# Optimization experiments

Measured on AMD Instinct MI355X. Metric: run time of the kernel, lower is better.

## Reference

```python
import jax, jax.numpy as jnp
import numpy as np

HIDDEN = 1024
HEADS = 16
HEAD = HIDDEN // HEADS


def setup_inputs() -> dict:
    key = jax.random.key(0)
    ks = jax.random.split(key, 6)
    B, T = 2, 2048
    x = jax.random.normal(ks[0], (B, T, HIDDEN), dtype=jnp.float32)
    mask = jnp.ones((T, T), dtype=jnp.float32)
    s = 1.0 / np.sqrt(HIDDEN)
    Wqkv = jax.random.normal(ks[1], (HIDDEN, 3 * HIDDEN), dtype=jnp.float32) * s
    bqkv = jnp.zeros((3 * HIDDEN,), dtype=jnp.float32)
    Wproj = jax.random.normal(ks[2], (HIDDEN, HIDDEN), dtype=jnp.float32) * s
    bproj = jnp.zeros((HIDDEN,), dtype=jnp.float32)
    return {"x": x, "mask": mask, "Wqkv": Wqkv, "bqkv": bqkv,
            "Wproj": Wproj, "bproj": bproj}


def reference(x, mask, Wqkv, bqkv, Wproj, bproj):
    B, T, C = x.shape
    qkv = x @ Wqkv + bqkv                      # [B,T,3C]
    q, k, v = jnp.split(qkv, 3, axis=-1)
    def heads(t):                              # [B,T,C] -> [B,H,T,D]
        return t.reshape(B, T, HEADS, HEAD).transpose(0, 2, 1, 3)
    q, k, v = heads(q), heads(k), heads(v)
    scores = jnp.einsum('bhqd,bhkd->bhqk', q, k) / np.sqrt(HEAD)
    scores = jnp.where(mask == 0, -jnp.inf, scores)
    attn = jax.nn.softmax(scores, axis=-1)
    out = jnp.einsum('bhqk,bhkd->bhqd', attn, v)
    out = out.transpose(0, 2, 1, 3).reshape(B, T, C)
    return out @ Wproj + bproj
```

## Files before the change

kernel.cpp:

```cpp
#include <hip/hip_runtime.h>
#include <stdint.h>

#define HID 1024
#define NH 16
#define HD 64
#define BATCH 2
#define SEQ 2048
#define MR (BATCH*SEQ)
#define NQKV (3*HID)

typedef __attribute__((ext_vector_type(8))) _Float16 h16x8;
typedef __attribute__((ext_vector_type(2))) __fp16 fp16x2;
typedef __attribute__((ext_vector_type(8))) unsigned short u16x8;
typedef __attribute__((ext_vector_type(4))) float f32x4;

#if __has_builtin(__builtin_amdgcn_exp2f)
#define EXP2(x) __builtin_amdgcn_exp2f(x)
#else
#define EXP2(x) exp2f(x)
#endif

static __device__ __forceinline__ unsigned short f2h(float f) {
  union { _Float16 h; unsigned short u; } v; v.h = (_Float16)f; return v.u;
}
static __device__ __forceinline__ unsigned pk2(float a, float b) {
  union { fp16x2 h; unsigned u; } v;
  v.h = __builtin_amdgcn_cvt_pkrtz(a, b);
  return v.u;
}

typedef const __attribute__((address_space(1))) unsigned int glb_u32;
typedef __attribute__((address_space(3))) unsigned int lds_u32;
static __device__ __forceinline__ void cp16(const void* g, void* l) {
  __builtin_amdgcn_global_load_lds((glb_u32*)g, (lds_u32*)l, 16, 0, 0);
}

#define QSCL (0.125f * 1.44269504f)

__global__ __launch_bounds__(256) void k_cvt(const float4* __restrict__ src,
                                             ushort4* __restrict__ dst) {
  int i = blockIdx.x * 256 + threadIdx.x;
  float4 v = src[i];
  ushort4 h;
  h.x = f2h(v.x); h.y = f2h(v.y); h.z = f2h(v.z); h.w = f2h(v.w);
  dst[i] = h;
}

__global__ __launch_bounds__(256) void k_transpose_h(const float* __restrict__ src,
                                                     int R, int C,
                                                     unsigned short* __restrict__ dst) {
  __shared__ float tile[32][33];
  int tx = threadIdx.x, ty = threadIdx.y;
  int col0 = blockIdx.x * 32, row0 = blockIdx.y * 32;
  #pragma unroll
  for (int i = 0; i < 32; i += 8)
    tile[ty + i][tx] = src[(size_t)(row0 + ty + i) * C + col0 + tx];
  __syncthreads();
  #pragma unroll
  for (int i = 0; i < 32; i += 8) {
    float v = tile[tx][ty + i];
    dst[(size_t)(col0 + ty + i) * R + row0 + tx] = f2h(v);
  }
}

__global__ __launch_bounds__(256) void k_maskbits(const float* __restrict__ mask,
                                                  unsigned long long* __restrict__ mb) {
  int gw = blockIdx.x * 4 + (threadIdx.x >> 6);
  int lane = threadIdx.x & 63;
  float v = mask[(size_t)gw * 64 + lane];
  unsigned long long b = __ballot(v != 0.f);
  if (lane == 0) mb[gw] = b;
}

__global__ __launch_bounds__(256) void k_gemm_qkv(const unsigned short* __restrict__ A,
                                                  const unsigned short* __restrict__ Bt,
                                                  const float* __restrict__ bias,
                                                  unsigned short* __restrict__ Qp,
                                                  unsigned short* __restrict__ Kp,
                                                  unsigned short* __restrict__ Vt) {
  const int K = HID;
  int tid = threadIdx.x;
  int wave = tid >> 6, lane = tid & 63, quad = lane >> 4, l16 = lane & 15;
  int wm = wave >> 1, wn = wave & 1;
  int x7 = l16 & 7;
  int m0 = blockIdx.y * 128, n0 = blockIdx.x * 128;
  __shared__ __align__(16) unsigned short As[128 * 64], Bs[128 * 64];
  f32x4 acc[4][4] = {};
  for (int k0 = 0; k0 < K; k0 += 64) {
    __syncthreads();
    #pragma unroll
    for (int i = 0; i < 4; i++) {
      int c = tid + i * 256;
      int r = c >> 3, sc = ((c ^ r) & 7) << 3;
      cp16(&A[(size_t)(m0 + r) * K + k0 + sc], &As[c << 3]);
      cp16(&Bt[(size_t)(n0 + r) * K + k0 + sc], &Bs[c << 3]);
    }
    __syncthreads();
    #pragma unroll
    for (int kc = 0; kc < 2; kc++) {
      h16x8 af[4], bf[4];
      #pragma unroll
      for (int i = 0; i < 4; i++) {
        af[i] = *(const h16x8*)&As[(wm * 64 + i * 16 + l16) * 64 + (((kc * 4 + quad) ^ x7) << 3)];
        bf[i] = *(const h16x8*)&Bs[(wn * 64 + i * 16 + l16) * 64 + (((kc * 4 + quad) ^ x7) << 3)];
      }
      #pragma unroll
      for (int i = 0; i < 4; i++)
        #pragma unroll
        for (int j = 0; j < 4; j++)
          acc[i][j] = __builtin_amdgcn_mfma_f32_16x16x32_f16(af[i], bf[j], acc[i][j], 0, 0, 0);
    }
  }
  #pragma unroll
  for (int j = 0; j < 4; j++) {
    int n = n0 + wn * 64 + j * 16 + l16;
    float bv = bias[n];
    int which = n >> 10;
    int rem = n & 1023;
    int h = rem >> 6, d = rem & 63;
    if (which == 2) {
      #pragma unroll
      for (int i = 0; i < 4; i++) {
        int m = m0 + wm * 64 + i * 16 + quad * 4;
        int b = m >> 11, t = m & 2047;
        uint2 tt;
        tt.x = pk2(acc[i][j][0] + bv, acc[i][j][1] + bv);
        tt.y = pk2(acc[i][j][2] + bv, acc[i][j][3] + bv);
        *(uint2*)&Vt[(size_t)(b * NH + h) * (SEQ * HD) + (size_t)d * SEQ + t] = tt;
      }
    } else {
      #pragma unroll
      for (int i = 0; i < 4; i++)
        #pragma unroll
        for (int r = 0; r < 4; r++) {
          int m = m0 + wm * 64 + i * 16 + quad * 4 + r;
          int b = m >> 11, t = m & 2047;
          float val = acc[i][j][r] + bv;
          int hb = b * NH + h;
          if (which == 0) Qp[(size_t)hb * (SEQ * HD) + (size_t)t * HD + d] = f2h(val * QSCL);
          else            Kp[(size_t)hb * (SEQ * HD) + (size_t)t * HD + d] = f2h(val);
        }
    }
  }
}

__global__ __launch_bounds__(256) void k_attn(const unsigned short* __restrict__ Qp,
                                              const unsigned short* __restrict__ Kp,
                                              const unsigned short* __restrict__ Vt,
                                              const unsigned long long* __restrict__ mb,
                                              unsigned short* __restrict__ AO) {
  int tid = threadIdx.x, wave = tid >> 6, lane = tid & 63, quad = lane >> 4, l16 = lane & 15;
  int bh = blockIdx.y, qbase = blockIdx.x * 64;
  const unsigned short* Qg = Qp + (size_t)bh * (SEQ * HD);
  const unsigned short* Kg = Kp + (size_t)bh * (SEQ * HD);
  const unsigned short* Vg = Vt + (size_t)bh * (SEQ * HD);
  __shared__ __align__(16) unsigned short smem[16896];
  unsigned short* Qs = smem;
  unsigned short* Ks = smem + 4096;
  unsigned short* Vs = smem + 8192;
  unsigned short* Ps = smem + 12288 + wave * (16 * 72);
  unsigned short* Os = smem + 4096;

  #pragma unroll
  for (int i = 0; i < 2; i++) {
    int c = tid + i * 256;
    int row = c >> 3, sc = ((c ^ row) & 7) << 3;
    cp16(&Qg[(size_t)(qbase + row) * HD + sc], &Qs[c << 3]);
  }
  int qrow = qbase + wave * 16 + l16;
  const unsigned long long* mrow = mb + (size_t)qrow * 32;
  f32x4 acc_o[4] = {};
  f32x4 acc_l = {};
  int x7 = l16 & 7;

  h16x8 vone;
  #pragma unroll
  for (int j = 0; j < 8; j++) vone[j] = (_Float16)1.0f;

  __syncthreads();
  h16x8 bq[2];
  #pragma unroll
  for (int kk = 0; kk < 2; kk++)
    bq[kk] = *(const h16x8*)&Qs[(wave * 16 + l16) * 64 + (((kk * 4 + quad) ^ x7) << 3)];

  for (int kt = 0; kt < 32; kt++) {
    int kbase = kt * 64;
    __syncthreads();
    #pragma unroll
    for (int i = 0; i < 2; i++) {
      int c = tid + i * 256;
      int row = c >> 3, sc = ((c ^ row) & 7) << 3;
      cp16(&Kg[(size_t)(kbase + row) * HD + sc], &Ks[c << 3]);
      cp16(&Vg[(size_t)row * SEQ + kbase + sc], &Vs[c << 3]);
    }
    unsigned long long w = mrow[kt];
    __syncthreads();
    f32x4 s[4] = {};
    #pragma unroll
    for (int nt = 0; nt < 4; nt++)
      #pragma unroll
      for (int kk = 0; kk < 2; kk++) {
        h16x8 a = *(const h16x8*)&Ks[(nt * 16 + l16) * 64 + (((kk * 4 + quad) ^ x7) << 3)];
        s[nt] = __builtin_amdgcn_mfma_f32_16x16x32_f16(a, bq[kk], s[nt], 0, 0, 0);
      }
    if (!__all(w == ~0ULL)) {
      #pragma unroll
      for (int nt = 0; nt < 4; nt++)
        #pragma unroll
        for (int r = 0; r < 4; r++)
          if (!((w >> (nt * 16 + quad * 4 + r)) & 1ULL)) s[nt][r] = -100.f;
    }
    #pragma unroll
    for (int nt = 0; nt < 4; nt++)
      #pragma unroll
      for (int r = 0; r < 4; r++) s[nt][r] = EXP2(s[nt][r]);
    #pragma unroll
    for (int nt = 0; nt < 4; nt++) {
      uint2 t;
      t.x = pk2(s[nt][0], s[nt][1]);
      t.y = pk2(s[nt][2], s[nt][3]);
      *(uint2*)&Ps[l16 * 72 + nt * 16 + quad * 4] = t;
    }
    h16x8 bp[2];
    #pragma unroll
    for (int kk = 0; kk < 2; kk++)
      bp[kk] = *(const h16x8*)&Ps[l16 * 72 + kk * 32 + quad * 8];
    acc_l = __builtin_amdgcn_mfma_f32_16x16x32_f16(vone, bp[0], acc_l, 0, 0, 0);
    acc_l = __builtin_amdgcn_mfma_f32_16x16x32_f16(vone, bp[1], acc_l, 0, 0, 0);
    #pragma unroll
    for (int nt = 0; nt < 4; nt++)
      #pragma unroll
      for (int kk = 0; kk < 2; kk++) {
        h16x8 a = *(const h16x8*)&Vs[(nt * 16 + l16) * 64 + (((kk * 4 + quad) ^ x7) << 3)];
        acc_o[nt] = __builtin_amdgcn_mfma_f32_16x16x32_f16(a, bp[kk], acc_o[nt], 0, 0, 0);
      }
  }
  float rl = 1.0f / acc_l[0];
  __syncthreads();
  #pragma unroll
  for (int nt = 0; nt < 4; nt++) {
    uint2 t;
    t.x = (unsigned)f2h(acc_o[nt][0] * rl) | ((unsigned)f2h(acc_o[nt][1] * rl) << 16);
    t.y = (unsigned)f2h(acc_o[nt][2] * rl) | ((unsigned)f2h(acc_o[nt][3] * rl) << 16);
    *(uint2*)&Os[(wave * 16 + l16) * 72 + nt * 16 + quad * 4] = t;
  }
  __syncthreads();
  int b = bh >> 4, h = bh & 15;
  #pragma unroll
  for (int i = 0; i < 2; i++) {
    int c = tid + i * 256;
    int row = c >> 3, co = (c & 7) << 3;
    u16x8 vv = *(const u16x8*)&Os[row * 72 + co];
    *(u16x8*)&AO[(size_t)(b * SEQ + qbase + row) * HID + h * HD + co] = vv;
  }
}

__global__ __launch_bounds__(256) void k_gemm_proj(const unsigned short* __restrict__ A,
                                                   const unsigned short* __restrict__ Bt,
                                                   const float* __restrict__ bias,
                                                   float* __restrict__ out) {
  const int K = HID;
  int tid = threadIdx.x;
  int wave = tid >> 6, lane = tid & 63, quad = lane >> 4, l16 = lane & 15;
  int wm = wave >> 1, wn = wave & 1;
  int x7 = l16 & 7;
  int m0 = blockIdx.y * 128, n0 = blockIdx.x * 128;
  __shared__ __align__(16) unsigned short As[128 * 64], Bs[128 * 64];
  f32x4 acc[4][4] = {};
  for (int k0 = 0; k0 < K; k0 += 64) {
    __syncthreads();
    #pragma unroll
    for (int i = 0; i < 4; i++) {
      int c = tid + i * 256;
      int r = c >> 3, sc = ((c ^ r) & 7) << 3;
      cp16(&A[(size_t)(m0 + r) * K + k0 + sc], &As[c << 3]);
      cp16(&Bt[(size_t)(n0 + r) * K + k0 + sc], &Bs[c << 3]);
    }
    __syncthreads();
    #pragma unroll
    for (int kc = 0; kc < 2; kc++) {
      h16x8 af[4], bf[4];
      #pragma unroll
      for (int i = 0; i < 4; i++) {
        af[i] = *(const h16x8*)&As[(wm * 64 + i * 16 + l16) * 64 + (((kc * 4 + quad) ^ x7) << 3)];
        bf[i] = *(const h16x8*)&Bs[(wn * 64 + i * 16 + l16) * 64 + (((kc * 4 + quad) ^ x7) << 3)];
      }
      #pragma unroll
      for (int i = 0; i < 4; i++)
        #pragma unroll
        for (int j = 0; j < 4; j++)
          acc[i][j] = __builtin_amdgcn_mfma_f32_16x16x32_f16(af[i], bf[j], acc[i][j], 0, 0, 0);
    }
  }
  #pragma unroll
  for (int j = 0; j < 4; j++) {
    int n = n0 + wn * 64 + j * 16 + l16;
    float bv = bias[n];
    #pragma unroll
    for (int i = 0; i < 4; i++)
      #pragma unroll
      for (int r = 0; r < 4; r++) {
        int m = m0 + wm * 64 + i * 16 + quad * 4 + r;
        out[(size_t)m * HID + n] = acc[i][j][r] + bv;
      }
  }
}

extern "C" void kernel_launch(void* const* d_in, const int* in_sizes, int n_in,
                              void* d_out, int out_size, void* d_ws, size_t ws_size,
                              hipStream_t stream) {
  const float* x     = (const float*)d_in[0];
  const float* mask  = (const float*)d_in[1];
  const float* Wqkv  = (const float*)d_in[2];
  const float* bqkv  = (const float*)d_in[3];
  const float* Wproj = (const float*)d_in[4];
  const float* bproj = (const float*)d_in[5];
  float* out = (float*)d_out;

  uint8_t* ws = (uint8_t*)d_ws;
  size_t off = 0;
  auto alloc = [&](size_t bytes) -> void* {
    void* p = (void*)(ws + off);
    off += (bytes + 255) & ~(size_t)255;
    return p;
  };
  unsigned short* xh   = (unsigned short*)alloc((size_t)MR * HID * 2);
  unsigned short* WqT  = (unsigned short*)alloc((size_t)NQKV * HID * 2);
  unsigned short* WpT  = (unsigned short*)alloc((size_t)HID * HID * 2);
  unsigned short* Qp   = (unsigned short*)alloc((size_t)BATCH * NH * SEQ * HD * 2);
  unsigned short* Kp   = (unsigned short*)alloc((size_t)BATCH * NH * SEQ * HD * 2);
  unsigned short* Vtp  = (unsigned short*)alloc((size_t)BATCH * NH * SEQ * HD * 2);
  unsigned short* AO   = (unsigned short*)alloc((size_t)MR * HID * 2);
  unsigned long long* mb = (unsigned long long*)alloc((size_t)SEQ * (SEQ / 64) * 8);

  k_cvt<<<MR * HID / 4 / 256, 256, 0, stream>>>((const float4*)x, (ushort4*)xh);
  k_transpose_h<<<dim3(NQKV / 32, HID / 32), dim3(32, 8), 0, stream>>>(Wqkv, HID, NQKV, WqT);
  k_transpose_h<<<dim3(HID / 32, HID / 32), dim3(32, 8), 0, stream>>>(Wproj, HID, HID, WpT);
  k_maskbits<<<SEQ * (SEQ / 64) / 4, 256, 0, stream>>>(mask, mb);
  k_gemm_qkv<<<dim3(NQKV / 128, MR / 128), 256, 0, stream>>>(xh, WqT, bqkv, Qp, Kp, Vtp);
  k_attn<<<dim3(SEQ / 64, BATCH * NH), 256, 0, stream>>>(Qp, Kp, Vtp, mb, AO);
  k_gemm_proj<<<dim3(HID / 128, MR / 128), 256, 0, stream>>>(AO, WpT, bproj, out);
}
```

Baseline: 229.3 us.

## Fuse prep kernels, double query rows per attention wave, narrow proj GEMM tiles

Merges the fp16 convert, both weight transposes and mask bit-packing into one launch, removing three kernel launches. Each attention wave now handles 32 query rows (128 per block), so every K/V fragment loaded from LDS feeds twice as many MFMAs, at the cost of more registers and half as many blocks. The projection GEMM uses 128x64 tiles to double its block count and fill more CUs on the small N=1024 output.

```diff
diff --git a/kernel.cpp b/kernel.cpp
--- a/kernel.cpp
+++ b/kernel.cpp
@@ -37,39 +37,42 @@
 
 #define QSCL (0.125f * 1.44269504f)
 
-__global__ __launch_bounds__(256) void k_cvt(const float4* __restrict__ src,
-                                             ushort4* __restrict__ dst) {
-  int i = blockIdx.x * 256 + threadIdx.x;
-  float4 v = src[i];
-  ushort4 h;
-  h.x = f2h(v.x); h.y = f2h(v.y); h.z = f2h(v.z); h.w = f2h(v.w);
-  dst[i] = h;
-}
-
-__global__ __launch_bounds__(256) void k_transpose_h(const float* __restrict__ src,
-                                                     int R, int C,
-                                                     unsigned short* __restrict__ dst) {
+__global__ __launch_bounds__(256) void k_prep(const float4* __restrict__ x4,
+                                              const float* __restrict__ mask,
+                                              const float* __restrict__ Wqkv,
+                                              const float* __restrict__ Wproj,
+                                              ushort4* __restrict__ xh,
+                                              unsigned short* __restrict__ WqT,
+                                              unsigned short* __restrict__ WpT,
+                                              unsigned long long* __restrict__ mb) {
   __shared__ float tile[32][33];
-  int tx = threadIdx.x, ty = threadIdx.y;
-  int col0 = blockIdx.x * 32, row0 = blockIdx.y * 32;
-  #pragma unroll
-  for (int i = 0; i < 32; i += 8)
-    tile[ty + i][tx] = src[(size_t)(row0 + ty + i) * C + col0 + tx];
-  __syncthreads();
-  #pragma unroll
-  for (int i = 0; i < 32; i += 8) {
-    float v = tile[tx][ty + i];
-    dst[(size_t)(col0 + ty + i) * R + row0 + tx] = f2h(v);
-  }
-}
-
-__global__ __launch_bounds__(256) void k_maskbits(const float* __restrict__ mask,
-                                                  unsigned long long* __restrict__ mb) {
-  int gw = blockIdx.x * 4 + (threadIdx.x >> 6);
-  int lane = threadIdx.x & 63;
-  float v = mask[(size_t)gw * 64 + lane];
-  unsigned long long b = __ballot(v != 0.f);
-  if (lane == 0) mb[gw] = b;
+  int blk = blockIdx.x, tid = threadIdx.x;
+  if (blk < 4096) {
+    int i = blk * 256 + tid;
+    float4 v = x4[i];
+    ushort4 h;
+    h.x = f2h(v.x); h.y = f2h(v.y); h.z = f2h(v.z); h.w = f2h(v.w);
+    xh[i] = h;
+  } else if (blk < 8192) {
+    const float* src; unsigned short* dst; int C, bx, by;
+    if (blk < 7168) { src = Wqkv;  dst = WqT; C = NQKV; int b2 = blk - 4096; bx = b2 % 96; by = b2 / 96; }
+    else            { src = Wproj; dst = WpT; C = HID;  int b2 = blk - 7168; bx = b2 & 31; by = b2 >> 5; }
+    int tx = tid & 31, ty = tid >> 5;
+    int col0 = bx * 32, row0 = by * 32;
+    #pragma unroll
+    for (int i = 0; i < 32; i += 8)
+      tile[ty + i][tx] = src[(size_t)(row0 + ty + i) * C + col0 + tx];
+    __syncthreads();
+    #pragma unroll
+    for (int i = 0; i < 32; i += 8)
+      dst[(size_t)(col0 + ty + i) * HID + row0 + tx] = f2h(tile[tx][ty + i]);
+  } else {
+    int gw = (blk - 8192) * 4 + (tid >> 6);
+    int lane = tid & 63;
+    float v = mask[(size_t)gw * 64 + lane];
+    unsigned long long b = __ballot(v != 0.f);
+    if (lane == 0) mb[gw] = b;
+  }
 }
 
 __global__ __launch_bounds__(256) void k_gemm_qkv(const unsigned short* __restrict__ A,
@@ -150,27 +153,28 @@
                                               const unsigned long long* __restrict__ mb,
                                               unsigned short* __restrict__ AO) {
   int tid = threadIdx.x, wave = tid >> 6, lane = tid & 63, quad = lane >> 4, l16 = lane & 15;
-  int bh = blockIdx.y, qbase = blockIdx.x * 64;
+  int bh = blockIdx.y, qbase = blockIdx.x * 128;
   const unsigned short* Qg = Qp + (size_t)bh * (SEQ * HD);
   const unsigned short* Kg = Kp + (size_t)bh * (SEQ * HD);
   const unsigned short* Vg = Vt + (size_t)bh * (SEQ * HD);
-  __shared__ __align__(16) unsigned short smem[16896];
+  __shared__ __align__(16) unsigned short smem[20992];
   unsigned short* Qs = smem;
-  unsigned short* Ks = smem + 4096;
-  unsigned short* Vs = smem + 8192;
-  unsigned short* Ps = smem + 12288 + wave * (16 * 72);
-  unsigned short* Os = smem + 4096;
-
-  #pragma unroll
-  for (int i = 0; i < 2; i++) {
+  unsigned short* Ks = smem + 8192;
+  unsigned short* Vs = smem + 12288;
+  unsigned short* Ps = smem + 16384 + wave * (16 * 72);
+  unsigned short* Os = smem;
+
+  #pragma unroll
+  for (int i = 0; i < 4; i++) {
     int c = tid + i * 256;
     int row = c >> 3, sc = ((c ^ row) & 7) << 3;
     cp16(&Qg[(size_t)(qbase + row) * HD + sc], &Qs[c << 3]);
   }
-  int qrow = qbase + wave * 16 + l16;
-  const unsigned long long* mrow = mb + (size_t)qrow * 32;
-  f32x4 acc_o[4] = {};
-  f32x4 acc_l = {};
+  int q0 = qbase + wave * 32 + l16;
+  const unsigned long long* mrow0 = mb + (size_t)q0 * 32;
+  const unsigned long long* mrow1 = mb + (size_t)(q0 + 16) * 32;
+  f32x4 acc_o[2][4] = {};
+  f32x4 acc_l[2] = {};
   int x7 = l16 & 7;
 
   h16x8 vone;
@@ -178,10 +182,12 @@
   for (int j = 0; j < 8; j++) vone[j] = (_Float16)1.0f;
 
   __syncthreads();
-  h16x8 bq[2];
-  #pragma unroll
-  for (int kk = 0; kk < 2; kk++)
-    bq[kk] = *(const h16x8*)&Qs[(wave * 16 + l16) * 64 + (((kk * 4 + quad) ^ x7) << 3)];
+  h16x8 bq[2][2];
+  #pragma unroll
+  for (int s = 0; s < 2; s++)
+    #pragma unroll
+    for (int kk = 0; kk < 2; kk++)
+      bq[s][kk] = *(const h16x8*)&Qs[(wave * 32 + s * 16 + l16) * 64 + (((kk * 4 + quad) ^ x7) << 3)];
 
   for (int kt = 0; kt < 32; kt++) {
     int kbase = kt * 64;
@@ -193,61 +199,100 @@
       cp16(&Kg[(size_t)(kbase + row) * HD + sc], &Ks[c << 3]);
       cp16(&Vg[(size_t)row * SEQ + kbase + sc], &Vs[c << 3]);
     }
-    unsigned long long w = mrow[kt];
-    __syncthreads();
-    f32x4 s[4] = {};
+    unsigned long long w0 = mrow0[kt], w1 = mrow1[kt];
+    __syncthreads();
+    h16x8 ka[4][2];
     #pragma unroll
     for (int nt = 0; nt < 4; nt++)
       #pragma unroll
+      for (int kk = 0; kk < 2; kk++)
+        ka[nt][kk] = *(const h16x8*)&Ks[(nt * 16 + l16) * 64 + (((kk * 4 + quad) ^ x7) << 3)];
+    f32x4 s0[4] = {}, s1[4] = {};
+    #pragma unroll
+    for (int nt = 0; nt < 4; nt++)
+      #pragma unroll
       for (int kk = 0; kk < 2; kk++) {
-        h16x8 a = *(const h16x8*)&Ks[(nt * 16 + l16) * 64 + (((kk * 4 + quad) ^ x7) << 3)];
-        s[nt] = __builtin_amdgcn_mfma_f32_16x16x32_f16(a, bq[kk], s[nt], 0, 0, 0);
-      }
-    if (!__all(w == ~0ULL)) {
+        s0[nt] = __builtin_amdgcn_mfma_f32_16x16x32_f16(ka[nt][kk], bq[0][kk], s0[nt], 0, 0, 0);
+        s1[nt] = __builtin_amdgcn_mfma_f32_16x16x32_f16(ka[nt][kk], bq[1][kk], s1[nt], 0, 0, 0);
+      }
+    if (!__all((w0 & w1) == ~0ULL)) {
       #pragma unroll
       for (int nt = 0; nt < 4; nt++)
         #pragma unroll
-        for (int r = 0; r < 4; r++)
-          if (!((w >> (nt * 16 + quad * 4 + r)) & 1ULL)) s[nt][r] = -100.f;
+        for (int r = 0; r < 4; r++) {
+          int bit = nt * 16 + quad * 4 + r;
+          if (!((w0 >> bit) & 1ULL)) s0[nt][r] = -100.f;
+          if (!((w1 >> bit) & 1ULL)) s1[nt][r] = -100.f;
+        }
     }
     #pragma unroll
     for (int nt = 0; nt < 4; nt++)
       #pragma unroll
-      for (int r = 0; r < 4; r++) s[nt][r] = EXP2(s[nt][r]);
+      for (int r = 0; r < 4; r++) {
+        s0[nt][r] = EXP2(s0[nt][r]);
+        s1[nt][r] = EXP2(s1[nt][r]);
+      }
+    h16x8 va[4][2];
+    #pragma unroll
+    for (int nt = 0; nt < 4; nt++)
+      #pragma unroll
+      for (int kk = 0; kk < 2; kk++)
+        va[nt][kk] = *(const h16x8*)&Vs[(nt * 16 + l16) * 64 + (((kk * 4 + quad) ^ x7) << 3)];
     #pragma unroll
     for (int nt = 0; nt < 4; nt++) {
       uint2 t;
-      t.x = pk2(s[nt][0], s[nt][1]);
-      t.y = pk2(s[nt][2], s[nt][3]);
+      t.x = pk2(s0[nt][0], s0[nt][1]);
+      t.y = pk2(s0[nt][2], s0[nt][3]);
       *(uint2*)&Ps[l16 * 72 + nt * 16 + quad * 4] = t;
     }
-    h16x8 bp[2];
-    #pragma unroll
-    for (int kk = 0; kk < 2; kk++)
-      bp[kk] = *(const h16x8*)&Ps[l16 * 72 + kk * 32 + quad * 8];
-    acc_l = __builtin_amdgcn_mfma_f32_16x16x32_f16(vone, bp[0], acc_l, 0, 0, 0);
-    acc_l = __builtin_amdgcn_mfma_f32_16x16x32_f16(vone, bp[1], acc_l, 0, 0, 0);
-    #pragma unroll
-    for (int nt = 0; nt < 4; nt++)
-      #pragma unroll
-      for (int kk = 0; kk < 2; kk++) {
-        h16x8 a = *(const h16x8*)&Vs[(nt * 16 + l16) * 64 + (((kk * 4 + quad) ^ x7) << 3)];
-        acc_o[nt] = __builtin_amdgcn_mfma_f32_16x16x32_f16(a, bp[kk], acc_o[nt], 0, 0, 0);
-      }
-  }
-  float rl = 1.0f / acc_l[0];
+    {
+      h16x8 bp0 = *(const h16x8*)&Ps[l16 * 72 + quad * 8];
+      h16x8 bp1 = *(const h16x8*)&Ps[l16 * 72 + 32 + quad * 8];
+      acc_l[0] = __builtin_amdgcn_mfma_f32_16x16x32_f16(vone, bp0, acc_l[0], 0, 0, 0);
+      acc_l[0] = __builtin_amdgcn_mfma_f32_16x16x32_f16(vone, bp1, acc_l[0], 0, 0, 0);
+      #pragma unroll
+      for (int nt = 0; nt < 4; nt++) {
+        acc_o[0][nt] = __builtin_amdgcn_mfma_f32_16x16x32_f16(va[nt][0], bp0, acc_o[0][nt], 0, 0, 0);
+        acc_o[0][nt] = __builtin_amdgcn_mfma_f32_16x16x32_f16(va[nt][1], bp1, acc_o[0][nt], 0, 0, 0);
+      }
+    }
+    #pragma unroll
+    for (int nt = 0; nt < 4; nt++) {
+      uint2 t;
+      t.x = pk2(s1[nt][0], s1[nt][1]);
+      t.y = pk2(s1[nt][2], s1[nt][3]);
+      *(uint2*)&Ps[l16 * 72 + nt * 16 + quad * 4] = t;
+    }
+    {
+      h16x8 bp0 = *(const h16x8*)&Ps[l16 * 72 + quad * 8];
+      h16x8 bp1 = *(const h16x8*)&Ps[l16 * 72 + 32 + quad * 8];
+      acc_l[1] = __builtin_amdgcn_mfma_f32_16x16x32_f16(vone, bp0, acc_l[1], 0, 0, 0);
+      acc_l[1] = __builtin_amdgcn_mfma_f32_16x16x32_f16(vone, bp1, acc_l[1], 0, 0, 0);
+      #pragma unroll
+      for (int nt = 0; nt < 4; nt++) {
+        acc_o[1][nt] = __builtin_amdgcn_mfma_f32_16x16x32_f16(va[nt][0], bp0, acc_o[1][nt], 0, 0, 0);
+        acc_o[1][nt] = __builtin_amdgcn_mfma_f32_16x16x32_f16(va[nt][1], bp1, acc_o[1][nt], 0, 0, 0);
+      }
+    }
+  }
+  float rl0 = 1.0f / acc_l[0][0];
+  float rl1 = 1.0f / acc_l[1][0];
   __syncthreads();
   #pragma unroll
   for (int nt = 0; nt < 4; nt++) {
     uint2 t;
-    t.x = (unsigned)f2h(acc_o[nt][0] * rl) | ((unsigned)f2h(acc_o[nt][1] * rl) << 16);
-    t.y = (unsigned)f2h(acc_o[nt][2] * rl) | ((unsigned)f2h(acc_o[nt][3] * rl) << 16);
-    *(uint2*)&Os[(wave * 16 + l16) * 72 + nt * 16 + quad * 4] = t;
+    t.x = (unsigned)f2h(acc_o[0][nt][0] * rl0) | ((unsigned)f2h(acc_o[0][nt][1] * rl0) << 16);
+    t.y = (unsigned)f2h(acc_o[0][nt][2] * rl0) | ((unsigned)f2h(acc_o[0][nt][3] * rl0) << 16);
+    *(uint2*)&Os[(wave * 32 + l16) * 72 + nt * 16 + quad * 4] = t;
+    uint2 u;
+    u.x = (unsigned)f2h(acc_o[1][nt][0] * rl1) | ((unsigned)f2h(acc_o[1][nt][1] * rl1) << 16);
+    u.y = (unsigned)f2h(acc_o[1][nt][2] * rl1) | ((unsigned)f2h(acc_o[1][nt][3] * rl1) << 16);
+    *(uint2*)&Os[(wave * 32 + 16 + l16) * 72 + nt * 16 + quad * 4] = u;
   }
   __syncthreads();
   int b = bh >> 4, h = bh & 15;
   #pragma unroll
-  for (int i = 0; i < 2; i++) {
+  for (int i = 0; i < 4; i++) {
     int c = tid + i * 256;
     int row = c >> 3, co = (c & 7) << 3;
     u16x8 vv = *(const u16x8*)&Os[row * 72 + co];
@@ -264,9 +309,9 @@
   int wave = tid >> 6, lane = tid & 63, quad = lane >> 4, l16 = lane & 15;
   int wm = wave >> 1, wn = wave & 1;
   int x7 = l16 & 7;
-  int m0 = blockIdx.y * 128, n0 = blockIdx.x * 128;
-  __shared__ __align__(16) unsigned short As[128 * 64], Bs[128 * 64];
-  f32x4 acc[4][4] = {};
+  int m0 = blockIdx.y * 128, n0 = blockIdx.x * 64;
+  __shared__ __align__(16) unsigned short As[128 * 64], Bs[64 * 64];
+  f32x4 acc[4][2] = {};
   for (int k0 = 0; k0 < K; k0 += 64) {
     __syncthreads();
     #pragma unroll
@@ -274,27 +319,33 @@
       int c = tid + i * 256;
       int r = c >> 3, sc = ((c ^ r) & 7) << 3;
       cp16(&A[(size_t)(m0 + r) * K + k0 + sc], &As[c << 3]);
+    }
+    #pragma unroll
+    for (int i = 0; i < 2; i++) {
+      int c = tid + i * 256;
+      int r = c >> 3, sc = ((c ^ r) & 7) << 3;
       cp16(&Bt[(size_t)(n0 + r) * K + k0 + sc], &Bs[c << 3]);
     }
     __syncthreads();
     #pragma unroll
     for (int kc = 0; kc < 2; kc++) {
-      h16x8 af[4], bf[4];
-      #pragma unroll
-      for (int i = 0; i < 4; i++) {
+      h16x8 af[4], bf[2];
+      #pragma unroll
+      for (int i = 0; i < 4; i++)
         af[i] = *(const h16x8*)&As[(wm * 64 + i * 16 + l16) * 64 + (((kc * 4 + quad) ^ x7) << 3)];
-        bf[i] = *(const h16x8*)&Bs[(wn * 64 + i * 16 + l16) * 64 + (((kc * 4 + quad) ^ x7) << 3)];
-      }
+      #pragma unroll
+      for (int j = 0; j < 2; j++)
+        bf[j] = *(const h16x8*)&Bs[(wn * 32 + j * 16 + l16) * 64 + (((kc * 4 + quad) ^ x7) << 3)];
       #pragma unroll
       for (int i = 0; i < 4; i++)
         #pragma unroll
-        for (int j = 0; j < 4; j++)
+        for (int j = 0; j < 2; j++)
           acc[i][j] = __builtin_amdgcn_mfma_f32_16x16x32_f16(af[i], bf[j], acc[i][j], 0, 0, 0);
     }
   }
   #pragma unroll
-  for (int j = 0; j < 4; j++) {
-    int n = n0 + wn * 64 + j * 16 + l16;
+  for (int j = 0; j < 2; j++) {
+    int n = n0 + wn * 32 + j * 16 + l16;
     float bv = bias[n];
     #pragma unroll
     for (int i = 0; i < 4; i++)
@@ -333,11 +384,9 @@
   unsigned short* AO   = (unsigned short*)alloc((size_t)MR * HID * 2);
   unsigned long long* mb = (unsigned long long*)alloc((size_t)SEQ * (SEQ / 64) * 8);
 
-  k_cvt<<<MR * HID / 4 / 256, 256, 0, stream>>>((const float4*)x, (ushort4*)xh);
-  k_transpose_h<<<dim3(NQKV / 32, HID / 32), dim3(32, 8), 0, stream>>>(Wqkv, HID, NQKV, WqT);
-  k_transpose_h<<<dim3(HID / 32, HID / 32), dim3(32, 8), 0, stream>>>(Wproj, HID, HID, WpT);
-  k_maskbits<<<SEQ * (SEQ / 64) / 4, 256, 0, stream>>>(mask, mb);
+  k_prep<<<24576, 256, 0, stream>>>((const float4*)x, mask, Wqkv, Wproj,
+                                    (ushort4*)xh, WqT, WpT, mb);
   k_gemm_qkv<<<dim3(NQKV / 128, MR / 128), 256, 0, stream>>>(xh, WqT, bqkv, Qp, Kp, Vtp);
-  k_attn<<<dim3(SEQ / 64, BATCH * NH), 256, 0, stream>>>(Qp, Kp, Vtp, mb, AO);
-  k_gemm_proj<<<dim3(HID / 128, MR / 128), 256, 0, stream>>>(AO, WpT, bproj, out);
-}
+  k_attn<<<dim3(SEQ / 128, BATCH * NH), 256, 0, stream>>>(Qp, Kp, Vtp, mb, AO);
+  k_gemm_proj<<<dim3(HID / 64, MR / 128), 256, 0, stream>>>(AO, WpT, bproj, out);
+}
```

Measured after the change: 219.2 us. -4.4%, faster.
